# Kernel tuning notes

Hardware: AMD Instinct MI355X
Metric: run time of the kernel (lower is better)

The kernel has to match this reference:

```python
import jax, jax.numpy as jnp
import numpy as np

CHI, CHO, K, PAD = 64, 64, 3, 1
EPS = 1e-5


def setup_inputs() -> dict:
    key = jax.random.key(0)
    ks = jax.random.split(key, 4)
    B, H, W = 4, 128, 128
    x = jax.random.normal(ks[0], (B, CHI, H, W), jnp.float32)
    # conv_offset: produces 3*dg*K*K = 27 channels (o1, o2, mask); init small so offsets are modest
    w_off = jax.random.normal(ks[1], (3 * K * K, CHI, K, K), jnp.float32) * 0.01
    b_off = jnp.zeros((3 * K * K,), jnp.float32)
    # main deformable conv weight/bias
    w = jax.random.normal(ks[2], (CHO, CHI, K, K), jnp.float32) * (1.0 / np.sqrt(CHI * K * K))
    b = jnp.zeros((CHO,), jnp.float32)
    # BatchNorm affine params
    gamma = jnp.ones((CHO,), jnp.float32)
    beta = jnp.zeros((CHO,), jnp.float32)
    return {"x": x, "w_off": w_off, "b_off": b_off, "w": w, "b": b, "gamma": gamma, "beta": beta}


def _deform_conv(x, w_off, b_off, w, b):
    B, C, H, W_ = x.shape
    # offset/mask prediction: plain 3x3 conv, pad 1 -> [B, 27, H, W]
    off = jax.lax.conv_general_dilated(
        x, w_off, (1, 1), ((PAD, PAD), (PAD, PAD)),
        dimension_numbers=("NCHW", "OIHW", "NCHW")) + b_off[None, :, None, None]
    o1, o2, m = jnp.split(off, 3, axis=1)
    # mmcv DCNv2: offset = cat(o1, o2) -> [B, 2*K*K, H, W], interleaved (dy, dx) per tap
    offset = jnp.concatenate([o1, o2], axis=1).reshape(B, K * K, 2, H, W_)
    mask = jax.nn.sigmoid(m)                      # [B, 9, H, W]
    dy, dx = offset[:, :, 0], offset[:, :, 1]     # [B, 9, H, W]

    ky, kx = jnp.meshgrid(jnp.arange(K), jnp.arange(K), indexing="ij")
    ky = ky.reshape(1, K * K, 1, 1).astype(x.dtype)
    kx = kx.reshape(1, K * K, 1, 1).astype(x.dtype)
    hh = jnp.arange(H, dtype=x.dtype).reshape(1, 1, H, 1)
    ww = jnp.arange(W_, dtype=x.dtype).reshape(1, 1, 1, W_)
    py = hh - PAD + ky + dy                       # sampling row coords [B,9,H,W]
    px = ww - PAD + kx + dx                       # sampling col coords [B,9,H,W]

    y0 = jnp.floor(py)
    x0 = jnp.floor(px)
    wy = py - y0
    wx = px - x0

    x_flat = x.reshape(B, C, H * W_)

    def gather(yi, xi):
        # bilinear corner gather with zero padding outside the feature map
        valid = ((yi >= 0) & (yi < H) & (xi >= 0) & (xi < W_)).astype(x.dtype)
        yc = jnp.clip(yi, 0, H - 1).astype(jnp.int32)
        xc = jnp.clip(xi, 0, W_ - 1).astype(jnp.int32)
        idx = (yc * W_ + xc).reshape(B, 1, -1)
        v = jnp.take_along_axis(x_flat, idx, axis=2).reshape(B, C, K * K, H, W_)
        return v * valid[:, None]

    v00 = gather(y0, x0)
    v01 = gather(y0, x0 + 1)
    v10 = gather(y0 + 1, x0)
    v11 = gather(y0 + 1, x0 + 1)

    wy_ = wy[:, None]
    wx_ = wx[:, None]
    val = (v00 * (1 - wy_) * (1 - wx_) + v01 * (1 - wy_) * wx_
           + v10 * wy_ * (1 - wx_) + v11 * wy_ * wx_)
    val = val * mask[:, None]                     # modulated sampling [B,C,9,H,W]

    out = jnp.einsum("bckhw,ock->bohw", val, w.reshape(CHO, CHI, K * K))
    return out + b[None, :, None, None]


def reference(x, w_off, b_off, w, b, gamma, beta):
    y = _deform_conv(x, w_off, b_off, w, b)
    # BatchNorm2d (training-mode forward: batch statistics, biased variance)
    mean = y.mean(axis=(0, 2, 3))
    var = y.var(axis=(0, 2, 3))
    yhat = (y - mean[None, :, None, None]) * jax.lax.rsqrt(var[None, :, None, None] + EPS)
    return jax.nn.relu(yhat * gamma[None, :, None, None] + beta[None, :, None, None])
```

## Files before the change

### kernel.cpp

```cpp
#include <hip/hip_runtime.h>
#include <math.h>

#define CHI 64
#define CHO 64
#define HH 128
#define WW 128
#define NB 4
#define KK 9
#define NOFF 27
#define EPSV 1e-5f
#define PLANE (HH * WW)
#define SP 72

typedef float f32x4 __attribute__((ext_vector_type(4)));
typedef short bf16x8 __attribute__((ext_vector_type(8)));
typedef unsigned int u32x4 __attribute__((ext_vector_type(4)));

__device__ __forceinline__ unsigned short f2bf(float f) {
    unsigned u = __float_as_uint(f);
    u += 0x7fff + ((u >> 16) & 1);
    return (unsigned short)(u >> 16);
}
__device__ __forceinline__ float bfl(unsigned u) { return __uint_as_float(u << 16); }
__device__ __forceinline__ float bfh(unsigned u) { return __uint_as_float(u & 0xffff0000u); }

__global__ __launch_bounds__(256) void prep_kernel(const float* __restrict__ x,
                                                   const float* __restrict__ w,
                                                   const float* __restrict__ w_off,
                                                   unsigned short* __restrict__ x_bf,
                                                   unsigned short* __restrict__ w_bf,
                                                   unsigned short* __restrict__ woA) {
    __shared__ unsigned short lt[128 * SP];
    if (blockIdx.x < 512) {
        const int id = blockIdx.x;
        const int b  = id >> 7;
        const int y  = id & 127;
        const int t  = threadIdx.x;
        const int ci = t >> 2, qx = t & 3;
        const float* src = x + ((size_t)(b * CHI + ci)) * PLANE + y * WW;
#pragma unroll
        for (int it = 0; it < 8; it++) {
            int xcol = (it * 4 + qx) * 4;
            float4 v = *(const float4*)(src + xcol);
            lt[(xcol + 0) * SP + ci] = f2bf(v.x);
            lt[(xcol + 1) * SP + ci] = f2bf(v.y);
            lt[(xcol + 2) * SP + ci] = f2bf(v.z);
            lt[(xcol + 3) * SP + ci] = f2bf(v.w);
        }
        __syncthreads();
        unsigned short* dst = x_bf + (size_t)id * (WW * 64);
#pragma unroll
        for (int it = 0; it < 4; it++) {
            int px  = it * 32 + (t >> 3);
            int ci8 = t & 7;
            u32x4 v = *(const u32x4*)&lt[px * SP + ci8 * 8];
            *(u32x4*)(dst + px * 64 + ci8 * 8) = v;
        }
    } else {
        int i = (blockIdx.x - 512) * 256 + threadIdx.x;
        {
            int j    = i & 7;
            int lane = (i >> 3) & 63;
            int ks   = (i >> 9) & 1;
            int ct   = (i >> 10) & 3;
            int kk   = i >> 12;
            int co   = ct * 16 + (lane & 15);
            int ci   = ks * 32 + ((lane >> 4) & 3) * 8 + j;
            w_bf[i]  = f2bf(w[(co * CHI + ci) * KK + kk]);
        }
        if (i < 18432) {
            int j    = i & 7;
            int lane = (i >> 3) & 63;
            int ct   = (i >> 9) & 1;
            int ks   = (i >> 10) & 1;
            int kk   = i >> 11;
            int c    = ct * 16 + (lane & 15);
            int ci   = ks * 32 + (lane >> 4) * 8 + j;
            woA[i]   = (c < NOFF) ? f2bf(w_off[(c * CHI + ci) * KK + kk]) : (unsigned short)0;
        }
    }
}

__global__ __launch_bounds__(256, 3) void deform_kernel(const unsigned short* __restrict__ x_bf,
                                                        const unsigned short* __restrict__ w_bf,
                                                        const unsigned short* __restrict__ woA,
                                                        const float* __restrict__ b_off,
                                                        float* __restrict__ out,
                                                        float* __restrict__ pstats) {
    const int id    = blockIdx.x;
    const int slot  = id & 7;
    const int b     = slot >> 1;
    const int rb    = id >> 3;
    const int h     = (slot & 1) * 64 + (rb >> 1);
    const int whalf = rb & 1;
    const int w0    = whalf * 64;
    const int tid   = threadIdx.x;
    const int lane  = tid & 63;
    const int wave  = __builtin_amdgcn_readfirstlane(tid >> 6);
    const int quad  = lane >> 4, pxin = lane & 15;
    const int pxl   = wave * 16 + pxin;

    __shared__ __align__(16) unsigned short xs[3 * 66 * SP];
    float* offs = (float*)xs;
    float* red  = (float*)(xs + 4096);

    const unsigned short* xb = x_bf + (size_t)b * (PLANE * 64);
#pragma unroll
    for (int ky = 0; ky < 3; ky++) {
        int hr = h - 1 + ky;
        for (int base = tid; base < 528; base += 256) {
            int col = base >> 3, ci8 = base & 7;
            int wc  = w0 - 1 + col;
            bool ok = ((unsigned)hr < HH) && ((unsigned)wc < WW);
            u32x4 v = {0u, 0u, 0u, 0u};
            if (ok) v = *(const u32x4*)(xb + ((size_t)(hr * WW + wc)) * 64 + ci8 * 8);
            *(u32x4*)&xs[(ky * 66 + col) * SP + ci8 * 8] = v;
        }
    }
    __syncthreads();

    f32x4 oacc0 = {0.f, 0.f, 0.f, 0.f};
    f32x4 oacc1 = {0.f, 0.f, 0.f, 0.f};
#pragma unroll 3
    for (int kk = 0; kk < KK; kk++) {
        const int ky = kk / 3, kx = kk - ky * 3;
#pragma unroll
        for (int ks = 0; ks < 2; ks++) {
            const bf16x8* wa = (const bf16x8*)woA + (size_t)((kk * 2 + ks) * 2) * 64;
            bf16x8 A0 = wa[lane];
            bf16x8 A1 = wa[64 + lane];
            bf16x8 B = *(const bf16x8*)&xs[(ky * 66 + wave * 16 + pxin + kx) * SP
                                           + ks * 32 + quad * 8];
            oacc0 = __builtin_amdgcn_mfma_f32_16x16x32_bf16(A0, B, oacc0, 0, 0, 0);
            oacc1 = __builtin_amdgcn_mfma_f32_16x16x32_bf16(A1, B, oacc1, 0, 0, 0);
        }
    }
    __syncthreads();

#pragma unroll
    for (int r = 0; r < 4; r++) {
        int c0 = quad * 4 + r;
        offs[pxl * 28 + c0] = oacc0[r];
        int c1 = 16 + quad * 4 + r;
        if (c1 < NOFF) offs[pxl * 28 + c1] = oacc1[r];
    }
    __syncthreads();

    f32x4 acc[4];
#pragma unroll
    for (int t = 0; t < 4; t++) acc[t] = (f32x4){0.f, 0.f, 0.f, 0.f};

    const int wpix = w0 + wave * 16 + pxin;
    const unsigned short* xbq = xb + quad * 8;

#pragma unroll 3
    for (int kk = 0; kk < KK; kk++) {
        const int ky = kk / 3, kx = kk - ky * 3;
        float dyv = offs[pxl * 28 + 2 * kk]     + b_off[2 * kk];
        float dxv = offs[pxl * 28 + 2 * kk + 1] + b_off[2 * kk + 1];
        float mov = offs[pxl * 28 + 18 + kk]    + b_off[18 + kk];

        float m   = 1.f / (1.f + __expf(-mov));
        float py  = (float)(h - 1 + ky) + dyv;
        float px_ = (float)(wpix - 1 + kx) + dxv;
        float fy0 = floorf(py), fx0 = floorf(px_);
        float wy = py - fy0, wx = px_ - fx0;
        int y0 = (int)fy0, x0 = (int)fx0;
        int y1 = y0 + 1, x1 = x0 + 1;
        bool vy0 = (unsigned)y0 < HH, vy1 = (unsigned)y1 < HH;
        bool vx0 = (unsigned)x0 < WW, vx1 = (unsigned)x1 < WW;
        float a00 = (vy0 && vx0) ? (1.f - wy) * (1.f - wx) * m : 0.f;
        float a01 = (vy0 && vx1) ? (1.f - wy) * wx * m : 0.f;
        float a10 = (vy1 && vx0) ? wy * (1.f - wx) * m : 0.f;
        float a11 = (vy1 && vx1) ? wy * wx * m : 0.f;
        int cy0 = min(max(y0, 0), HH - 1), cy1 = min(max(y1, 0), HH - 1);
        int cx0 = min(max(x0, 0), WW - 1), cx1 = min(max(x1, 0), WW - 1);
        const unsigned o00 = ((unsigned)(cy0 * WW + cx0)) << 6;
        const unsigned o01 = ((unsigned)(cy0 * WW + cx1)) << 6;
        const unsigned o10 = ((unsigned)(cy1 * WW + cx0)) << 6;
        const unsigned o11 = ((unsigned)(cy1 * WW + cx1)) << 6;

        u32x4 g00a = *(const u32x4*)(xbq + o00);
        u32x4 g01a = *(const u32x4*)(xbq + o01);
        u32x4 g10a = *(const u32x4*)(xbq + o10);
        u32x4 g11a = *(const u32x4*)(xbq + o11);
        u32x4 g00b = *(const u32x4*)(xbq + o00 + 32);
        u32x4 g01b = *(const u32x4*)(xbq + o01 + 32);
        u32x4 g10b = *(const u32x4*)(xbq + o10 + 32);
        u32x4 g11b = *(const u32x4*)(xbq + o11 + 32);

        const bf16x8* wb = (const bf16x8*)w_bf + (size_t)(kk * 8) * 64;
        bf16x8 A[8];
#pragma unroll
        for (int q = 0; q < 8; q++) A[q] = wb[q * 64 + lane];

        bf16x8 B0, B1;
#pragma unroll
        for (int d = 0; d < 4; d++) {
            float tl = a00 * bfl(g00a[d]) + a01 * bfl(g01a[d])
                     + a10 * bfl(g10a[d]) + a11 * bfl(g11a[d]);
            float th = a00 * bfh(g00a[d]) + a01 * bfh(g01a[d])
                     + a10 * bfh(g10a[d]) + a11 * bfh(g11a[d]);
            B0[2 * d]     = (short)f2bf(tl);
            B0[2 * d + 1] = (short)f2bf(th);
            float ul = a00 * bfl(g00b[d]) + a01 * bfl(g01b[d])
                     + a10 * bfl(g10b[d]) + a11 * bfl(g11b[d]);
            float uh = a00 * bfh(g00b[d]) + a01 * bfh(g01b[d])
                     + a10 * bfh(g10b[d]) + a11 * bfh(g11b[d]);
            B1[2 * d]     = (short)f2bf(ul);
            B1[2 * d + 1] = (short)f2bf(uh);
        }

#pragma unroll
        for (int t = 0; t < 4; t++) {
            acc[t] = __builtin_amdgcn_mfma_f32_16x16x32_bf16(A[t * 2 + 0], B0, acc[t], 0, 0, 0);
            acc[t] = __builtin_amdgcn_mfma_f32_16x16x32_bf16(A[t * 2 + 1], B1, acc[t], 0, 0, 0);
        }
    }

#pragma unroll
    for (int t = 0; t < 4; t++) {
#pragma unroll
        for (int r = 0; r < 4; r++) {
            int co = t * 16 + quad * 4 + r;
            out[(((size_t)b * CHO + co) * HH + h) * WW + w0 + wave * 16 + pxin] =
                acc[t][r];
        }
    }

#pragma unroll
    for (int t = 0; t < 4; t++) {
#pragma unroll
        for (int r = 0; r < 4; r++) {
            float s  = acc[t][r];
            float s2 = s * s;
#pragma unroll
            for (int mk = 1; mk < 16; mk <<= 1) {
                s  += __shfl_xor(s, mk, 64);
                s2 += __shfl_xor(s2, mk, 64);
            }
            if (pxin == 0) {
                int co = t * 16 + quad * 4 + r;
                red[(0 * 4 + wave) * 64 + co] = s;
                red[(1 * 4 + wave) * 64 + co] = s2;
            }
        }
    }
    __syncthreads();
    if (tid < 128) {
        int part = tid >> 6, idx = tid & 63;
        float v = red[(part * 4 + 0) * 64 + idx] + red[(part * 4 + 1) * 64 + idx]
                + red[(part * 4 + 2) * 64 + idx] + red[(part * 4 + 3) * 64 + idx];
        pstats[(size_t)(part * 64 + idx) * 1024 + id] = v;
    }
}

__global__ __launch_bounds__(256) void reduce_kernel(const float* __restrict__ pstats,
                                                     const float* __restrict__ bias,
                                                     float* __restrict__ stats) {
    const int co = blockIdx.x;
    const float* ps  = pstats + (size_t)co * 1024;
    const float* ps2 = pstats + (size_t)(64 + co) * 1024;
    float s = 0.f, s2 = 0.f;
    for (int i = threadIdx.x; i < 1024; i += 256) {
        s  += ps[i];
        s2 += ps2[i];
    }
#pragma unroll
    for (int o = 32; o > 0; o >>= 1) {
        s  += __shfl_down(s, o, 64);
        s2 += __shfl_down(s2, o, 64);
    }
    __shared__ float ls[8];
    int lane = threadIdx.x & 63, wv = threadIdx.x >> 6;
    if (lane == 0) { ls[wv] = s; ls[4 + wv] = s2; }
    __syncthreads();
    if (threadIdx.x == 0) {
        float S = ls[0] + ls[1] + ls[2] + ls[3];
        float S2 = ls[4] + ls[5] + ls[6] + ls[7];
        float bi = bias[co];
        stats[co]      = S + 65536.f * bi;
        stats[64 + co] = S2 + 2.f * bi * S + 65536.f * bi * bi;
    }
}

__global__ __launch_bounds__(256) void bn_kernel(float* __restrict__ y,
                                                 const float* __restrict__ bias,
                                                 const float* __restrict__ stats,
                                                 const float* __restrict__ gamma,
                                                 const float* __restrict__ beta) {
    size_t base = (size_t)blockIdx.x * 1024;
    int co = (int)((base >> 14) & 63);
    const float inv_n = 1.f / 65536.f;
    float mean = stats[co] * inv_n;
    float var  = stats[64 + co] * inv_n - mean * mean;
    float sc = gamma[co] * rsqrtf(var + EPSV);
    float sh = beta[co] - mean * sc;
    sh += bias[co] * sc;
    float4* p = (float4*)(y + base);
    float4 v = p[threadIdx.x];
    v.x = fmaxf(fmaf(v.x, sc, sh), 0.f);
    v.y = fmaxf(fmaf(v.y, sc, sh), 0.f);
    v.z = fmaxf(fmaf(v.z, sc, sh), 0.f);
    v.w = fmaxf(fmaf(v.w, sc, sh), 0.f);
    p[threadIdx.x] = v;
}

extern "C" void kernel_launch(void* const* d_in, const int* in_sizes, int n_in,
                              void* d_out, int out_size, void* d_ws, size_t ws_size,
                              hipStream_t stream) {
    const float* x     = (const float*)d_in[0];
    const float* w_off = (const float*)d_in[1];
    const float* b_off = (const float*)d_in[2];
    const float* wmat  = (const float*)d_in[3];
    const float* bvec  = (const float*)d_in[4];
    const float* gamma = (const float*)d_in[5];
    const float* beta  = (const float*)d_in[6];
    float* out = (float*)d_out;

    char* ws = (char*)d_ws;
    float* stats          = (float*)ws;
    unsigned short* w_bf  = (unsigned short*)(ws + 1024);
    unsigned short* woA   = (unsigned short*)(ws + 74752);
    unsigned short* x_bf  = (unsigned short*)(ws + 139264);
    float* pstats         = (float*)(ws + 8527872);

    prep_kernel<<<656, 256, 0, stream>>>(x, wmat, w_off, x_bf, w_bf, woA);
    deform_kernel<<<1024, 256, 0, stream>>>(x_bf, w_bf, woA, b_off, out, pstats);
    reduce_kernel<<<64, 256, 0, stream>>>(pstats, bvec, stats);
    bn_kernel<<<4096, 256, 0, stream>>>(out, bvec, stats, gamma, beta);
}
```

Measured before the change: 154.2 us.

## Fuse BN stats reduction into normalize kernel and split deform shared buffers

Merges the per-channel partial-stats reduction and the BN+ReLU apply into one kernel: each of 512 blocks redundantly reduces its channel's 1024 partials, then normalizes a half-plane segment. This removes one kernel launch and the stats round-trip through global memory. The deform kernel gets separate shared arrays for offsets and reductions, which drops one barrier between the offset MFMA loop and the offset stores. Its launch bound is raised to 4 blocks per CU, which may force register spills. The extra shared memory per block may also limit occupancy.

Result: faster. 138.1 us (-10.4%).

```diff
diff --git a/kernel.cpp b/kernel.cpp
--- a/kernel.cpp
+++ b/kernel.cpp
@@ -81,7 +81,7 @@
     }
 }
 
-__global__ __launch_bounds__(256, 3) void deform_kernel(const unsigned short* __restrict__ x_bf,
+__global__ __launch_bounds__(256, 4) void deform_kernel(const unsigned short* __restrict__ x_bf,
                                                         const unsigned short* __restrict__ w_bf,
                                                         const unsigned short* __restrict__ woA,
                                                         const float* __restrict__ b_off,
@@ -101,8 +101,8 @@
     const int pxl   = wave * 16 + pxin;
 
     __shared__ __align__(16) unsigned short xs[3 * 66 * SP];
-    float* offs = (float*)xs;
-    float* red  = (float*)(xs + 4096);
+    __shared__ float offs[64 * 27];
+    __shared__ float red[512];
 
     const unsigned short* xb = x_bf + (size_t)b * (PLANE * 64);
 #pragma unroll
@@ -135,14 +135,13 @@
             oacc1 = __builtin_amdgcn_mfma_f32_16x16x32_bf16(A1, B, oacc1, 0, 0, 0);
         }
     }
-    __syncthreads();
 
 #pragma unroll
     for (int r = 0; r < 4; r++) {
         int c0 = quad * 4 + r;
-        offs[pxl * 28 + c0] = oacc0[r];
+        offs[pxl * 27 + c0] = oacc0[r];
         int c1 = 16 + quad * 4 + r;
-        if (c1 < NOFF) offs[pxl * 28 + c1] = oacc1[r];
+        if (c1 < NOFF) offs[pxl * 27 + c1] = oacc1[r];
     }
     __syncthreads();
 
@@ -156,9 +155,9 @@
 #pragma unroll 3
     for (int kk = 0; kk < KK; kk++) {
         const int ky = kk / 3, kx = kk - ky * 3;
-        float dyv = offs[pxl * 28 + 2 * kk]     + b_off[2 * kk];
-        float dxv = offs[pxl * 28 + 2 * kk + 1] + b_off[2 * kk + 1];
-        float mov = offs[pxl * 28 + 18 + kk]    + b_off[18 + kk];
+        float dyv = offs[pxl * 27 + 2 * kk]     + b_off[2 * kk];
+        float dxv = offs[pxl * 27 + 2 * kk + 1] + b_off[2 * kk + 1];
+        float mov = offs[pxl * 27 + 18 + kk]    + b_off[18 + kk];
 
         float m   = 1.f / (1.f + __expf(-mov));
         float py  = (float)(h - 1 + ky) + dyv;
@@ -255,55 +254,50 @@
     }
 }
 
-__global__ __launch_bounds__(256) void reduce_kernel(const float* __restrict__ pstats,
-                                                     const float* __restrict__ bias,
-                                                     float* __restrict__ stats) {
-    const int co = blockIdx.x;
+__global__ __launch_bounds__(256) void statsbn_kernel(float* __restrict__ y,
+                                                      const float* __restrict__ pstats,
+                                                      const float* __restrict__ bias,
+                                                      const float* __restrict__ gamma,
+                                                      const float* __restrict__ beta) {
+    const int co  = blockIdx.x & 63;
+    const int seg = blockIdx.x >> 6;
+    const int t   = threadIdx.x;
+
     const float* ps  = pstats + (size_t)co * 1024;
     const float* ps2 = pstats + (size_t)(64 + co) * 1024;
-    float s = 0.f, s2 = 0.f;
-    for (int i = threadIdx.x; i < 1024; i += 256) {
-        s  += ps[i];
-        s2 += ps2[i];
-    }
+    float s  = ps[t]  + ps[t + 256]  + ps[t + 512]  + ps[t + 768];
+    float s2 = ps2[t] + ps2[t + 256] + ps2[t + 512] + ps2[t + 768];
 #pragma unroll
     for (int o = 32; o > 0; o >>= 1) {
         s  += __shfl_down(s, o, 64);
         s2 += __shfl_down(s2, o, 64);
     }
     __shared__ float ls[8];
-    int lane = threadIdx.x & 63, wv = threadIdx.x >> 6;
+    int lane = t & 63, wv = t >> 6;
     if (lane == 0) { ls[wv] = s; ls[4 + wv] = s2; }
     __syncthreads();
-    if (threadIdx.x == 0) {
-        float S = ls[0] + ls[1] + ls[2] + ls[3];
-        float S2 = ls[4] + ls[5] + ls[6] + ls[7];
-        float bi = bias[co];
-        stats[co]      = S + 65536.f * bi;
-        stats[64 + co] = S2 + 2.f * bi * S + 65536.f * bi * bi;
-    }
-}
-
-__global__ __launch_bounds__(256) void bn_kernel(float* __restrict__ y,
-                                                 const float* __restrict__ bias,
-                                                 const float* __restrict__ stats,
-                                                 const float* __restrict__ gamma,
-                                                 const float* __restrict__ beta) {
-    size_t base = (size_t)blockIdx.x * 1024;
-    int co = (int)((base >> 14) & 63);
+    float S0 = ls[0] + ls[1] + ls[2] + ls[3];
+    float S2 = ls[4] + ls[5] + ls[6] + ls[7];
+    float bi = bias[co];
+    float Sb  = S0 + 65536.f * bi;
+    float S2b = S2 + 2.f * bi * S0 + 65536.f * bi * bi;
     const float inv_n = 1.f / 65536.f;
-    float mean = stats[co] * inv_n;
-    float var  = stats[64 + co] * inv_n - mean * mean;
+    float mean = Sb * inv_n;
+    float var  = S2b * inv_n - mean * mean;
     float sc = gamma[co] * rsqrtf(var + EPSV);
-    float sh = beta[co] - mean * sc;
-    sh += bias[co] * sc;
-    float4* p = (float4*)(y + base);
-    float4 v = p[threadIdx.x];
-    v.x = fmaxf(fmaf(v.x, sc, sh), 0.f);
-    v.y = fmaxf(fmaf(v.y, sc, sh), 0.f);
-    v.z = fmaxf(fmaf(v.z, sc, sh), 0.f);
-    v.w = fmaxf(fmaf(v.w, sc, sh), 0.f);
-    p[threadIdx.x] = v;
+    float sh = beta[co] - mean * sc + bi * sc;
+
+    const int b = seg >> 1, half = seg & 1;
+    float4* p = (float4*)(y + ((size_t)(b * CHO + co)) * PLANE + half * 8192);
+#pragma unroll
+    for (int it = 0; it < 8; it++) {
+        float4 v = p[it * 256 + t];
+        v.x = fmaxf(fmaf(v.x, sc, sh), 0.f);
+        v.y = fmaxf(fmaf(v.y, sc, sh), 0.f);
+        v.z = fmaxf(fmaf(v.z, sc, sh), 0.f);
+        v.w = fmaxf(fmaf(v.w, sc, sh), 0.f);
+        p[it * 256 + t] = v;
+    }
 }
 
 extern "C" void kernel_launch(void* const* d_in, const int* in_sizes, int n_in,
@@ -319,7 +313,6 @@
     float* out = (float*)d_out;
 
     char* ws = (char*)d_ws;
-    float* stats          = (float*)ws;
     unsigned short* w_bf  = (unsigned short*)(ws + 1024);
     unsigned short* woA   = (unsigned short*)(ws + 74752);
     unsigned short* x_bf  = (unsigned short*)(ws + 139264);
@@ -327,6 +320,5 @@
 
     prep_kernel<<<656, 256, 0, stream>>>(x, wmat, w_off, x_bf, w_bf, woA);
     deform_kernel<<<1024, 256, 0, stream>>>(x_bf, w_bf, woA, b_off, out, pstats);
-    reduce_kernel<<<64, 256, 0, stream>>>(pstats, bvec, stats);
-    bn_kernel<<<4096, 256, 0, stream>>>(out, bvec, stats, gamma, beta);
-}
+    statsbn_kernel<<<512, 256, 0, stream>>>(out, pstats, bvec, gamma, beta);
+}
```
